# Optimization experiments

Hardware: AMD Instinct MI355X
Metric: run time of the kernel (lower is better)

Reference implementation:

```python
import jax, jax.numpy as jnp
import numpy as np

ANG = 5   # angular resolution (u = v = 5, n = 25 views)
CH = 64   # input channels
D = 2 * CH  # spa_dim + ang_dim + fre_dim = c/2 + c/2 + c = 128
NEG = -1e15


def _l2(x):
    # torch F.normalize over the contraction axis (last axis of folded layout)
    n = jnp.sqrt(jnp.sum(x * x, axis=-1, keepdims=True))
    return x / jnp.maximum(n, 1e-12)


def setup_inputs() -> dict:
    key = jax.random.key(0)
    ks = jax.random.split(key, 8)
    b, c, n, h, w = 4, CH, ANG * ANG, 32, 32
    d = D
    return {
        "x_lf": jax.random.normal(ks[0], (b, c, n, h, w), jnp.float32),
        "x_hf": jax.random.normal(ks[1], (b, c, n, h, w), jnp.float32),
        "W_in": jax.random.normal(ks[2], (c, d), jnp.float32) / np.sqrt(c).astype(np.float32),
        "W_kv": jax.random.normal(ks[3], (c, d), jnp.float32) / np.sqrt(c).astype(np.float32),
        "ln_g": jnp.ones((d,), jnp.float32),
        "ln_b": jnp.zeros((d,), jnp.float32),
        "W_m1": jax.random.normal(ks[4], (d, d), jnp.float32) / np.sqrt(d).astype(np.float32),
        "W_m2": jax.random.normal(ks[5], (d, d), jnp.float32) / np.sqrt(d).astype(np.float32),
        "W_out": jax.random.normal(ks[6], (d, c), jnp.float32) / np.sqrt(d).astype(np.float32),
    }


def _attend(fold, unfold, tq, tk, tv):
    # fold(t): (b, cc, u*v, h, w) -> (b, M, K); k/v use the same folding
    qf = _l2(fold(tq))            # q normalized over contraction axis
    kf = _l2(fold(tk))            # k normalized over contraction axis (dim=-2 of k^T)
    vf = fold(tv)
    att = jnp.einsum('bmk,bnk->bmn', qf, kf)   # (b, M, M)
    M = att.shape[-1]
    tril = jnp.tril(jnp.ones((M, M), bool))    # causal mask over folded axis
    att = jax.nn.softmax(jnp.where(tril, att, NEG), axis=-1)
    return unfold(att @ vf) + tv               # residual with token_v


def reference(x_lf, x_hf, W_in, W_kv, ln_g, ln_b, W_m1, W_m2, W_out):
    b, c, n, h, w = x_hf.shape
    u = v = ANG
    d = W_in.shape[1]

    def to_tokens(x, W):
        # 'b c (u v) h w -> (b u v) (h w) c' ; Linear ; back to 'b d (u v) h w'
        xt = x.reshape(b, c, u, v, h, w).transpose(0, 2, 3, 4, 5, 1).reshape(b * u * v, h * w, c)
        y = xt @ W
        return y.reshape(b, u, v, h, w, d).transpose(0, 5, 1, 2, 3, 4).reshape(b, d, u * v, h, w)

    q = to_tokens(x_hf, W_in)
    kv = to_tokens(x_lf, W_kv)
    cq = d // 4
    sf_q, af_q, sa_q = q[:, :cq], q[:, cq:2 * cq], q[:, 2 * cq:]
    sf_kv, af_kv, sa_kv = kv[:, :cq], kv[:, cq:2 * cq], kv[:, 2 * cq:]

    # SpatialFrequency: 'b c (u v) h w -> b (c h) (w u v)'
    def sf_fold(t):
        cc = t.shape[1]
        return t.reshape(b, cc, u, v, h, w).transpose(0, 1, 4, 5, 2, 3).reshape(b, cc * h, w * u * v)
    def sf_unfold(t):
        cc = t.shape[1] // h
        return t.reshape(b, cc, h, w, u, v).transpose(0, 1, 4, 5, 2, 3).reshape(b, cc, u * v, h, w)

    # AngularFrequency: 'b c (u v) h w -> b (c u) (h v w)'
    def af_fold(t):
        cc = t.shape[1]
        return t.reshape(b, cc, u, v, h, w).transpose(0, 1, 2, 4, 3, 5).reshape(b, cc * u, h * v * w)
    def af_unfold(t):
        cc = t.shape[1] // u
        return t.reshape(b, cc, u, h, v, w).transpose(0, 1, 2, 4, 3, 5).reshape(b, cc, u * v, h, w)

    # SpatialAngular: 'b c (u v) h w -> b (h u) (c v w)'
    def sa_fold(t):
        cc = t.shape[1]
        return t.reshape(b, cc, u, v, h, w).transpose(0, 4, 2, 1, 3, 5).reshape(b, h * u, cc * v * w)
    def sa_unfold(t):
        cc = t.shape[2] // (v * w) if t.ndim == 3 else t.shape[1]
        t = t.reshape(b, h, u, cc, v, w)
        return t.transpose(0, 3, 2, 4, 1, 5).reshape(b, cc, u * v, h, w)

    sf = _attend(sf_fold, sf_unfold, sf_q, sf_kv, sf_kv)
    af = _attend(af_fold, af_unfold, af_q, af_kv, af_kv)
    sa = _attend(sa_fold, sa_unfold, sa_q, sa_kv, sa_kv)

    cat = jnp.concatenate([sf, af, sa], axis=1)  # (b, d, n, h, w)
    ct = cat.reshape(b, d, u, v, h, w).transpose(0, 2, 3, 4, 5, 1).reshape(b * u * v, h * w, d)

    # c_mlp: LayerNorm -> Linear -> ReLU -> Linear (dropout is identity in eval)
    mu = jnp.mean(ct, axis=-1, keepdims=True)
    var = jnp.mean(jnp.square(ct - mu), axis=-1, keepdims=True)
    ln = (ct - mu) / jnp.sqrt(var + 1e-5) * ln_g + ln_b
    mlp = jax.nn.relu(ln @ W_m1) @ W_m2
    out_t = (mlp + ct) @ W_out  # residual then output projection

    out = out_t.reshape(b, u, v, h, w, -1).transpose(0, 5, 1, 2, 3, 4).reshape(b, -1, u * v, h, w)
    return out
```

## Files before the change

kernel.cpp:

```cpp
#include <hip/hip_runtime.h>

#define NSP   25600
#define HWC   1024

typedef __attribute__((ext_vector_type(8))) short bf8;
typedef __attribute__((ext_vector_type(4))) float f4;
#define MFMA(a,b,c) __builtin_amdgcn_mfma_f32_16x16x32_bf16(a, b, c, 0, 0, 0)
typedef unsigned short u16;

__device__ __forceinline__ u16 f2b(float f) {
    union { float f; unsigned u; } v; v.f = f;
    unsigned r = v.u + 0x7fffu + ((v.u >> 16) & 1u);
    return (u16)(r >> 16);
}
__device__ __forceinline__ float b2f(u16 h) {
    union { unsigned u; float f; } v; v.u = ((unsigned)h) << 16;
    return v.f;
}

__device__ __forceinline__ long row_base(int att, int b, int m) {
    if (att == 0) { int cc = m >> 5, h = m & 31;   return ((long)(b*128 + cc))*NSP + h*32; }
    else if (att == 1) { int cc = m / 5, u = m - cc*5; return ((long)(b*128 + 32 + cc))*NSP + u*5120; }
    else { int h = m / 5, u = m - h*5;            return ((long)(b*128 + 64))*NSP + u*5120 + h*32; }
}
__device__ __forceinline__ long chunk_off(int att, int kc) {
    if (att == 0) return (long)kc * 1024;
    else if (att == 1) return (long)kc * 32;
    else { int cc = kc / 5, v = kc - cc*5; return (long)cc*NSP + v*1024; }
}

__global__ __launch_bounds__(256) void k_prep(
        const float* __restrict__ Wi, const float* __restrict__ Wk,
        const float* __restrict__ W1, const float* __restrict__ W2,
        const float* __restrict__ Wo, u16* __restrict__ wbt) {
    int e = blockIdx.x * 256 + threadIdx.x;
    const float* src; int base, K, N;
    if (e < 8192)       { src = Wi; base = 0;     K = 64;  N = 128; }
    else if (e < 16384) { src = Wk; base = 8192;  K = 64;  N = 128; }
    else if (e < 32768) { src = W1; base = 16384; K = 128; N = 128; }
    else if (e < 49152) { src = W2; base = 32768; K = 128; N = 128; }
    else                { src = Wo; base = 49152; K = 128; N = 64;  }
    int local = e - base, n = local / K, k = local - n * K;
    wbt[e] = f2b(src[k * N + n]);
}

__global__ __launch_bounds__(256) void k_prep2(
        const float* __restrict__ W2, const float* __restrict__ Wo,
        u16* __restrict__ w2o) {
    int e = blockIdx.x * 256 + threadIdx.x;
    int o = e >> 7, k = e & 127;
    float s = 0.f;
    for (int n = 0; n < 128; ++n) s += W2[k * 128 + n] * Wo[n * 64 + o];
    w2o[e] = f2b(s);
}

__global__ __launch_bounds__(256) void k_tokens(
        const float* __restrict__ x_hf, const float* __restrict__ x_lf,
        const u16* __restrict__ wbt,
        u16* __restrict__ qb, u16* __restrict__ kvb) {
    int s0 = blockIdx.x * 64, b = blockIdx.y, which = blockIdx.z;
    const float* x  = which ? x_lf : x_hf;
    const u16* Wb = wbt + (which ? 8192 : 0);
    u16* out = which ? kvb : qb;
    __shared__ u16 Axs[64 * 72];
    __shared__ u16 Wl [128 * 72];
    int tid = threadIdx.x;
    for (int g = tid; g < 1024; g += 256) {
        int d = g >> 3, c8 = (g & 7) * 8;
        *(bf8*)&Wl[d * 72 + c8] = *(const bf8*)(Wb + d * 64 + c8);
    }
    for (int g = tid; g < 1024; g += 256) {
        int s = g & 63, c4 = (g >> 6) * 4;
        long xb = ((long)(b * 64 + c4)) * NSP + s0 + s;
        ushort4 pk;
        pk.x = f2b(x[xb]);
        pk.y = f2b(x[xb + NSP]);
        pk.z = f2b(x[xb + 2 * NSP]);
        pk.w = f2b(x[xb + 3 * NSP]);
        *(ushort4*)&Axs[s * 72 + c4] = pk;
    }
    __syncthreads();
    int w = tid >> 6, l = tid & 63, quad = l >> 4, col = l & 15;
    f4 z = {0.f, 0.f, 0.f, 0.f};
    f4 acc[8]; for (int i = 0; i < 8; ++i) acc[i] = z;
#pragma unroll
    for (int kc = 0; kc < 2; ++kc) {
        bf8 a = *(bf8*)&Axs[(w * 16 + col) * 72 + kc * 32 + quad * 8];
#pragma unroll
        for (int nt = 0; nt < 8; ++nt) {
            bf8 bb = *(bf8*)&Wl[(nt * 16 + col) * 72 + kc * 32 + quad * 8];
            acc[nt] = MFMA(a, bb, acc[nt]);
        }
    }
#pragma unroll
    for (int nt = 0; nt < 8; ++nt) {
        int d = nt * 16 + col;
        long base = ((long)(b * 128 + d)) * NSP + s0 + w * 16 + quad * 4;
        ushort4 pk;
        pk.x = f2b(acc[nt][0]); pk.y = f2b(acc[nt][1]);
        pk.z = f2b(acc[nt][2]); pk.w = f2b(acc[nt][3]);
        *(ushort4*)(out + base) = pk;
    }
}

__global__ __launch_bounds__(256) void k_vt_norms(
        const u16* __restrict__ qb, const u16* __restrict__ kvb,
        u16* __restrict__ vt0, u16* __restrict__ vt1, u16* __restrict__ vt2,
        float* __restrict__ nq, float* __restrict__ nk) {
    int x = blockIdx.x, b = blockIdx.y;
    int tid = threadIdx.x;
    __shared__ u16 T[128 * 36];
    if (x < 200) {
        int kc = x >> 3, pt = (x & 7) * 128;
        long co = (long)kc * 1024;
#pragma unroll
        for (int i = 0; i < 4; ++i) {
            int idx = i * 256 + tid;
            int r = idx >> 3, fq = (idx & 7) * 4;
            ushort4 e = *(const ushort4*)(kvb + row_base(0, b, pt + r) + co + fq);
            *(ushort4*)&T[r * 36 + fq] = e;
        }
        __syncthreads();
#pragma unroll
        for (int i = 0; i < 4; ++i) {
            int idx = i * 256 + tid;
            int f = idx >> 5, p4 = (idx & 31) * 4;
            ushort4 pk;
            pk.x = T[(p4    ) * 36 + f];
            pk.y = T[(p4 + 1) * 36 + f];
            pk.z = T[(p4 + 2) * 36 + f];
            pk.w = T[(p4 + 3) * 36 + f];
            *(ushort4*)(vt0 + (((long)b * 25 + kc) * 32 + f) * 1024 + pt + p4) = pk;
        }
    } else if (x < 2600) {
        int att, kc, pt, KC; u16* vt;
        if (x < 1000) { int x2 = x - 200;  att = 1; kc = x2 / 5; pt = (x2 - kc * 5) * 32; KC = 160; vt = vt1; }
        else          { int x3 = x - 1000; att = 2; kc = x3 / 5; pt = (x3 - kc * 5) * 32; KC = 320; vt = vt2; }
        long co = chunk_off(att, kc);
        {
            int r = tid >> 3, fq = (tid & 7) * 4;
            ushort4 e = *(const ushort4*)(kvb + row_base(att, b, pt + r) + co + fq);
            *(ushort4*)&T[r * 36 + fq] = e;
        }
        __syncthreads();
        {
            int f = tid >> 3, p4 = (tid & 7) * 4;
            ushort4 pk;
            pk.x = T[(p4    ) * 36 + f];
            pk.y = T[(p4 + 1) * 36 + f];
            pk.z = T[(p4 + 2) * 36 + f];
            pk.w = T[(p4 + 3) * 36 + f];
            *(ushort4*)(vt + (((long)b * KC + kc) * 32 + f) * 160 + pt + p4) = pk;
        }
    } else {
        int x2 = x - 2600;
        int which = x2 >= 336;
        int g = which ? x2 - 336 : x2;
        int att, m0, KC;
        if (g < 256)      { att = 0; m0 = g * 4;         KC = 25;  }
        else if (g < 296) { att = 1; m0 = (g - 256) * 4; KC = 160; }
        else              { att = 2; m0 = (g - 296) * 4; KC = 320; }
        const u16* src = which ? kvb : qb;
        float* dst = which ? nk : nq;
        int w = tid >> 6, lane = tid & 63;
        int m = m0 + w;
        long base = row_base(att, b, m);
        int K = KC * 32;
        float s = 0.f;
        for (int k8 = lane * 8; k8 < K; k8 += 512) {
            bf8 v = *(const bf8*)(src + base + chunk_off(att, k8 >> 5) + (k8 & 31));
#pragma unroll
            for (int j = 0; j < 8; ++j) { float f = b2f(((u16*)&v)[j]); s += f * f; }
        }
        for (int o = 32; o >= 1; o >>= 1) s += __shfl_xor(s, o);
        if (lane == 0) {
            int off = (att == 0) ? b * 1024 + m
                                 : ((att == 1) ? 4096 : 4736) + b * 160 + m;
            dst[off] = fmaxf(sqrtf(s), 1e-12f);
        }
    }
}

__global__ __launch_bounds__(256) void k_sgemm_all(
        const u16* __restrict__ qb, const u16* __restrict__ kvb,
        const float* __restrict__ nq, const float* __restrict__ nk,
        u16* __restrict__ Sb, float* __restrict__ Spart) {
    __shared__ float lds[4096];
    int x = blockIdx.x, b = blockIdx.y;
    int tid = threadIdx.x, w = tid >> 6, l = tid & 63, quad = l >> 4, col = l & 15;
    if (x < 136) {
        u16* Qs = (u16*)lds;
        u16* Ks = Qs + 64 * 40;
        int t = x, i = 0;
        while (t >= (i + 1) * (i + 2) / 2) ++i;
        int j = t - i * (i + 1) / 2;
        int mt = i * 64, nt = j * 64;
        int srow = tid >> 2, g = tid & 3;
        f4 z = {0.f, 0.f, 0.f, 0.f};
        f4 acc[4]; for (int q = 0; q < 4; ++q) acc[q] = z;
        for (int kc = 0; kc < 25; ++kc) {
            long co = (long)kc * 1024;
            {
                int m = mt + srow;
                *(bf8*)&Qs[srow * 40 + g * 8] =
                    *(const bf8*)(qb + ((long)(b*128 + (m >> 5)))*NSP + (m & 31)*32 + co + g*8);
                int n = nt + srow;
                *(bf8*)&Ks[srow * 40 + g * 8] =
                    *(const bf8*)(kvb + ((long)(b*128 + (n >> 5)))*NSP + (n & 31)*32 + co + g*8);
            }
            __syncthreads();
            bf8 a = *(bf8*)&Qs[(w * 16 + col) * 40 + quad * 8];
#pragma unroll
            for (int t2 = 0; t2 < 4; ++t2) {
                bf8 bb = *(bf8*)&Ks[(t2 * 16 + col) * 40 + quad * 8];
                acc[t2] = MFMA(a, bb, acc[t2]);
            }
            __syncthreads();
        }
#pragma unroll
        for (int t2 = 0; t2 < 4; ++t2)
#pragma unroll
            for (int r = 0; r < 4; ++r) {
                int m = mt + w * 16 + quad * 4 + r, n = nt + t2 * 16 + col;
                float v = (n <= m) ? acc[t2][r] / (nq[b*1024 + m] * nk[b*1024 + n]) : 0.f;
                Sb[((long)b * 1024 + m) * 1024 + n] = f2b(v);
            }
    } else {
        int x2 = x - 136;
        int t = x2 % 15, y = x2 / 15;
        int att, split, nsplit; float* base;
        if (y < 10) { att = 1; split = y;      nsplit = 10; base = Spart; }
        else        { att = 2; split = y - 10; nsplit = 20; base = Spart + 614400; }
        int i = 0;
        while (t >= (i + 1) * (i + 2) / 2) ++i;
        int j = t - i * (i + 1) / 2;
        int mt = i * 32, nt = j * 32;
        long rm0 = row_base(att, b, mt + col),      rm1 = row_base(att, b, mt + 16 + col);
        long rn0 = row_base(att, b, nt + col),      rn1 = row_base(att, b, nt + 16 + col);
        int ko = quad * 8;
        f4 z = {0.f, 0.f, 0.f, 0.f};
        f4 a00 = z, a01 = z, a10 = z, a11 = z;
#pragma unroll
        for (int s = 0; s < 4; ++s) {
            int kc = split * 16 + w * 4 + s;
            long co = chunk_off(att, kc);
            bf8 qa0 = *(const bf8*)(qb + rm0 + co + ko);
            bf8 qa1 = *(const bf8*)(qb + rm1 + co + ko);
            bf8 kb0 = *(const bf8*)(kvb + rn0 + co + ko);
            bf8 kb1 = *(const bf8*)(kvb + rn1 + co + ko);
            a00 = MFMA(qa0, kb0, a00); a01 = MFMA(qa0, kb1, a01);
            a10 = MFMA(qa1, kb0, a10); a11 = MFMA(qa1, kb1, a11);
        }
        float* my = lds + w * 1024;
#pragma unroll
        for (int r = 0; r < 4; ++r) {
            my[(quad * 4 + r) * 32 + col]            = a00[r];
            my[(quad * 4 + r) * 32 + 16 + col]       = a01[r];
            my[(16 + quad * 4 + r) * 32 + col]       = a10[r];
            my[(16 + quad * 4 + r) * 32 + 16 + col]  = a11[r];
        }
        __syncthreads();
        float* dst = base + ((long)((b * 15 + t) * nsplit + split)) * 1024;
        for (int e = tid; e < 1024; e += 256)
            dst[e] = lds[e] + lds[1024 + e] + lds[2048 + e] + lds[3072 + e];
    }
}

__global__ __launch_bounds__(256) void k_softmax_all(
        const u16* __restrict__ Sb, u16* __restrict__ Pb,
        const float* __restrict__ Spart, const float* __restrict__ nq,
        const float* __restrict__ nk, u16* __restrict__ Pb12) {
    int xb = blockIdx.x, b = blockIdx.y, tid = threadIdx.x;
    if (xb < 256) {
        int w = tid >> 6, lane = tid & 63;
        int m = xb * 4 + w;
        const u16* row = Sb + ((long)b * 1024 + m) * 1024;
        u16* pr = Pb + ((long)b * 1024 + m) * 1024;
        int e0 = lane * 16;
        bf8 x0 = *(const bf8*)(row + e0);
        bf8 x1 = *(const bf8*)(row + e0 + 8);
        float v[16];
#pragma unroll
        for (int j = 0; j < 8; ++j) { v[j] = b2f(((u16*)&x0)[j]); v[8 + j] = b2f(((u16*)&x1)[j]); }
        float mx = -1e30f;
#pragma unroll
        for (int j = 0; j < 16; ++j) if (e0 + j <= m) mx = fmaxf(mx, v[j]);
#pragma unroll
        for (int o = 32; o >= 1; o >>= 1) mx = fmaxf(mx, __shfl_xor(mx, o));
        float s = 0.f;
#pragma unroll
        for (int j = 0; j < 16; ++j) {
            float e = (e0 + j <= m) ? __expf(v[j] - mx) : 0.f;
            v[j] = e; s += e;
        }
#pragma unroll
        for (int o = 32; o >= 1; o >>= 1) s += __shfl_xor(s, o);
        float inv = 1.f / s;
        bf8 o0, o1;
#pragma unroll
        for (int j = 0; j < 8; ++j) {
            ((u16*)&o0)[j] = f2b(v[j] * inv);
            ((u16*)&o1)[j] = f2b(v[8 + j] * inv);
        }
        *(bf8*)(pr + e0) = o0;
        *(bf8*)(pr + e0 + 8) = o1;
    } else {
        int x = xb - 256;
        int att = (x < 160) ? 1 : 2;
        int m = (att == 1) ? x : x - 160;
        int nsplit = (att == 1) ? 10 : 20;
        const float* base = (att == 1) ? Spart : Spart + 614400;
        int noff = (att == 1) ? 4096 : 4736;
        u16* P = Pb12 + ((att == 1) ? 0 : 102400);
        int i = m >> 5, ro = (m & 31) * 32;
        int n = tid;
        bool act = (n <= m) && (n < 160);
        float myv = 0.f;
        if (act) {
            int t = i * (i + 1) / 2 + (n >> 5);
            const float* src = base + ((long)((b * 15 + t) * nsplit)) * 1024 + ro + (n & 31);
            float s = 0.f;
            for (int sp = 0; sp < nsplit; ++sp) s += src[(long)sp * 1024];
            myv = s / (nq[noff + b * 160 + m] * nk[noff + b * 160 + n]);
        }
        __shared__ float red[256];
        red[tid] = act ? myv : -1e30f; __syncthreads();
        for (int w = 128; w >= 1; w >>= 1) {
            if (tid < w) red[tid] = fmaxf(red[tid], red[tid + w]);
            __syncthreads();
        }
        float mx = red[0]; __syncthreads();
        float e = act ? __expf(myv - mx) : 0.f;
        red[tid] = e; __syncthreads();
        for (int w = 128; w >= 1; w >>= 1) {
            if (tid < w) red[tid] += red[tid + w];
            __syncthreads();
        }
        float inv = 1.f / red[0];
        if (n < 160) P[((long)b * 160 + m) * 160 + n] = f2b(e * inv);
    }
}

__global__ __launch_bounds__(256) void k_ogemm_all(
        const u16* __restrict__ Pb, const u16* __restrict__ vt0,
        const u16* __restrict__ Pb12, const u16* __restrict__ vt1,
        const u16* __restrict__ vt2, const u16* __restrict__ kvb,
        u16* __restrict__ catb) {
    __shared__ __align__(16) u16 lds[64 * 72 + 32 * 72];
    int x = blockIdx.x, b = blockIdx.y;
    int tid = threadIdx.x, w = tid >> 6, l = tid & 63, quad = l >> 4, col = l & 15;
    if (x < 400) {
        int mtt = x & 15, kc = x >> 4;
        int mt = mtt * 64;
        long co = (long)kc * 1024;
        const u16* vtc = vt0 + ((long)b * 25 + kc) * 32 * 1024;
        u16* Ps = lds;
        u16* Vs = lds + 64 * 72;
        f4 z = {0.f, 0.f, 0.f, 0.f};
        f4 acc[2]; acc[0] = z; acc[1] = z;
        for (int s = 0; s <= mtt; ++s) {
            int p0 = s * 64;
#pragma unroll
            for (int i = 0; i < 2; ++i) {
                int idx = i * 256 + tid;
                int row = idx >> 3, c8 = (idx & 7) * 8;
                *(bf8*)&Ps[row * 72 + c8] =
                    *(const bf8*)(Pb + ((long)(b * 1024 + mt + row)) * 1024 + p0 + c8);
            }
            {
                int f = tid >> 3, p8 = (tid & 7) * 8;
                *(bf8*)&Vs[f * 72 + p8] =
                    *(const bf8*)(vtc + (long)f * 1024 + p0 + p8);
            }
            __syncthreads();
            bf8 a0 = *(bf8*)&Ps[(w * 16 + col) * 72 + quad * 8];
            bf8 a1 = *(bf8*)&Ps[(w * 16 + col) * 72 + 32 + quad * 8];
#pragma unroll
            for (int t2 = 0; t2 < 2; ++t2) {
                bf8 b0 = *(bf8*)&Vs[(t2 * 16 + col) * 72 + quad * 8];
                bf8 b1 = *(bf8*)&Vs[(t2 * 16 + col) * 72 + 32 + quad * 8];
                acc[t2] = MFMA(a0, b0, acc[t2]);
                acc[t2] = MFMA(a1, b1, acc[t2]);
            }
            __syncthreads();
        }
#pragma unroll
        for (int t2 = 0; t2 < 2; ++t2)
#pragma unroll
            for (int r = 0; r < 4; ++r) {
                int m = mt + w * 16 + quad * 4 + r, f = t2 * 16 + col;
                long adr = ((long)(b * 128 + (m >> 5))) * NSP + (m & 31) * 32 + co + f;
                catb[adr] = f2b(acc[t2][r] + b2f(kvb[adr]));
            }
    } else {
        int x2 = x - 400;
        int att = (x2 < 320) ? 1 : 2;
        int ft  = (att == 1) ? x2 : x2 - 320;
        int KC  = (att == 1) ? 160 : 320;
        const u16* vt = (att == 1) ? vt1 : vt2;
        const u16* Prow = Pb12 + ((att == 1) ? 0 : 102400) + (long)b * 160 * 160;
        u16* Vs = lds;
        for (int g = tid; g < 320; g += 256) {
            int fl = g / 20, p8 = (g % 20) * 8;
            int fglob = ft * 16 + fl;
            int kc = fglob >> 5, fr = fglob & 31;
            *(bf8*)&Vs[fl * 168 + p8] =
                *(const bf8*)(vt + (((long)b * KC + kc) * 32 + fr) * 160 + p8);
        }
        __syncthreads();
        int fglob = ft * 16 + col;
        int kcf = fglob >> 5, fi = fglob & 31;
        long cbase = chunk_off(att, kcf) + fi;
        f4 z = {0.f, 0.f, 0.f, 0.f};
        for (int j = 0; j < 3; ++j) {
            int mi = w + 4 * j;
            if (mi >= 10) break;
            int nkk = (mi >> 1) + 1;
            f4 acc = z;
#pragma unroll 5
            for (int kk = 0; kk < nkk; ++kk) {
                bf8 a  = *(const bf8*)(Prow + (mi * 16 + col) * 160 + kk * 32 + quad * 8);
                bf8 bb = *(bf8*)&Vs[col * 168 + kk * 32 + quad * 8];
                acc = MFMA(a, bb, acc);
            }
#pragma unroll
            for (int r = 0; r < 4; ++r) {
                int m = mi * 16 + quad * 4 + r;
                long adr = row_base(att, b, m) + cbase;
                catb[adr] = f2b(acc[r] + b2f(kvb[adr]));
            }
        }
    }
}

__global__ __launch_bounds__(256) void k_mlp_fused(
        const u16* __restrict__ catb, const float* __restrict__ g,
        const float* __restrict__ be, const u16* __restrict__ wbt,
        const u16* __restrict__ w2o, float* __restrict__ out) {
    int x = blockIdx.x, tid = threadIdx.x;
    int tt = x * 64;
    int bn = tt >> 10, hwt = tt & 1023;
    int b = bn / 25, uv = bn - b * 25;
    __shared__ u16 CT[64 * 136];
    __shared__ u16 Wt[128 * 136];
    __shared__ float gl[128], bl[128], mu_s[64], rs_s[64];
    int w = tid >> 6, l = tid & 63, quad = l >> 4, col = l & 15;
    const u16* src = catb + (long)b * 128 * NSP + (long)uv * HWC + hwt;
#pragma unroll
    for (int i = 0; i < 4; ++i) {
        int gi = i * 256 + tid;
        int d = gi >> 3, hw8 = (gi & 7) * 8;
        bf8 v = *(const bf8*)(src + (long)d * NSP + hw8);
#pragma unroll
        for (int j = 0; j < 8; ++j) CT[(hw8 + j) * 136 + d] = ((u16*)&v)[j];
    }
    {
        const u16* Wob = wbt + 49152;
        for (int q = tid; q < 1024; q += 256) {
            int o = q >> 4, k8 = (q & 15) * 8;
            *(bf8*)&Wt[o * 136 + k8] = *(const bf8*)(Wob + o * 128 + k8);
        }
    }
    if (tid < 128) { gl[tid] = g[tid]; bl[tid] = be[tid]; }
    __syncthreads();
    f4 z = {0.f, 0.f, 0.f, 0.f};
    f4 acc_o[4]; for (int i = 0; i < 4; ++i) acc_o[i] = z;
#pragma unroll
    for (int kc = 0; kc < 4; ++kc) {
        bf8 a = *(bf8*)&CT[(w * 16 + col) * 136 + kc * 32 + quad * 8];
#pragma unroll
        for (int nt = 0; nt < 4; ++nt) {
            bf8 bb = *(bf8*)&Wt[(nt * 16 + col) * 136 + kc * 32 + quad * 8];
            acc_o[nt] = MFMA(a, bb, acc_o[nt]);
        }
    }
    {
        int tk = w * 16 + (l >> 2), dg = (l & 3) * 32;
        float s = 0.f, s2 = 0.f;
#pragma unroll
        for (int q = 0; q < 4; ++q) {
            bf8 vv = *(bf8*)&CT[tk * 136 + dg + q * 8];
#pragma unroll
            for (int j = 0; j < 8; ++j) { float f = b2f(((u16*)&vv)[j]); s += f; s2 += f * f; }
        }
        s += __shfl_xor(s, 1); s2 += __shfl_xor(s2, 1);
        s += __shfl_xor(s, 2); s2 += __shfl_xor(s2, 2);
        if ((l & 3) == 0) {
            float m = s * (1.f / 128.f);
            float var = s2 * (1.f / 128.f) - m * m;
            mu_s[tk] = m; rs_s[tk] = rsqrtf(var + 1e-5f);
        }
    }
    __syncthreads();
    for (int q = tid; q < 1024; q += 256) {
        int row = q >> 4, k8 = (q & 15) * 8;
        bf8 cv = *(bf8*)&CT[row * 136 + k8];
        float m = mu_s[row], rs = rs_s[row];
        bf8 av;
#pragma unroll
        for (int j = 0; j < 8; ++j)
            ((u16*)&av)[j] = f2b((b2f(((u16*)&cv)[j]) - m) * rs * gl[k8 + j] + bl[k8 + j]);
        *(bf8*)&CT[row * 136 + k8] = av;
    }
    {
        const u16* W1b = wbt + 16384;
        for (int q = tid; q < 2048; q += 256) {
            int n = q >> 4, k8 = (q & 15) * 8;
            *(bf8*)&Wt[n * 136 + k8] = *(const bf8*)(W1b + n * 128 + k8);
        }
    }
    __syncthreads();
    f4 acc_h[8]; for (int i = 0; i < 8; ++i) acc_h[i] = z;
#pragma unroll
    for (int kc = 0; kc < 4; ++kc) {
        bf8 a = *(bf8*)&CT[(w * 16 + col) * 136 + kc * 32 + quad * 8];
#pragma unroll
        for (int nt = 0; nt < 8; ++nt) {
            bf8 bb = *(bf8*)&Wt[(nt * 16 + col) * 136 + kc * 32 + quad * 8];
            acc_h[nt] = MFMA(a, bb, acc_h[nt]);
        }
    }
    __syncthreads();
#pragma unroll
    for (int nt = 0; nt < 8; ++nt)
#pragma unroll
        for (int r = 0; r < 4; ++r) {
            int row = w * 16 + quad * 4 + r, n = nt * 16 + col;
            CT[row * 136 + n] = f2b(fmaxf(acc_h[nt][r], 0.f));
        }
    for (int q = tid; q < 1024; q += 256) {
        int o = q >> 4, k8 = (q & 15) * 8;
        *(bf8*)&Wt[o * 136 + k8] = *(const bf8*)(w2o + o * 128 + k8);
    }
    __syncthreads();
#pragma unroll
    for (int kc = 0; kc < 4; ++kc) {
        bf8 a = *(bf8*)&CT[(w * 16 + col) * 136 + kc * 32 + quad * 8];
#pragma unroll
        for (int nt = 0; nt < 4; ++nt) {
            bf8 bb = *(bf8*)&Wt[(nt * 16 + col) * 136 + kc * 32 + quad * 8];
            acc_o[nt] = MFMA(a, bb, acc_o[nt]);
        }
    }
    int hw = hwt + w * 16 + quad * 4;
#pragma unroll
    for (int nt = 0; nt < 4; ++nt) {
        int o = nt * 16 + col;
        float4 pk = {acc_o[nt][0], acc_o[nt][1], acc_o[nt][2], acc_o[nt][3]};
        *(float4*)(out + ((long)((b * 64 + o) * 25 + uv)) * 1024 + hw) = pk;
    }
}

extern "C" void kernel_launch(void* const* d_in, const int* in_sizes, int n_in,
                              void* d_out, int out_size, void* d_ws, size_t ws_size,
                              hipStream_t stream) {
    const float* x_lf = (const float*)d_in[0];
    const float* x_hf = (const float*)d_in[1];
    const float* W_in = (const float*)d_in[2];
    const float* W_kv = (const float*)d_in[3];
    const float* ln_g = (const float*)d_in[4];
    const float* ln_b = (const float*)d_in[5];
    const float* W_m1 = (const float*)d_in[6];
    const float* W_m2 = (const float*)d_in[7];
    const float* W_ot = (const float*)d_in[8];
    float* out = (float*)d_out;

    float* ws = (float*)d_ws;
    u16*   qb    = (u16*)ws;
    u16*   kvb   = (u16*)(ws + 6553600);
    u16*   catb  = (u16*)(ws + 13107200);
    u16*   Sb    = (u16*)(ws + 26214400);
    u16*   Pb    = (u16*)(ws + 28311552);
    u16*   Pb12  = (u16*)(ws + 30408704);
    float* Spart = ws + 30511104;
    float* nq    = ws + 32354304;
    float* nk    = ws + 32359680;
    u16*   w2ob  = (u16*)(ws + 32365056);
    u16*   vt0   = (u16*)(ws + 32569856);
    u16*   vt1   = (u16*)(ws + 34208256);
    u16*   vt2   = (u16*)(ws + 35846656);
    u16*   wbt   = (u16*)(ws + 39123456);

    k_prep<<<dim3(224), 256, 0, stream>>>(W_in, W_kv, W_m1, W_m2, W_ot, wbt);
    k_prep2<<<dim3(32), 256, 0, stream>>>(W_m2, W_ot, w2ob);

    k_tokens<<<dim3(400, 4, 2), 256, 0, stream>>>(x_hf, x_lf, wbt, qb, kvb);

    k_vt_norms<<<dim3(3272, 4), 256, 0, stream>>>(qb, kvb, vt0, vt1, vt2, nq, nk);

    k_sgemm_all<<<dim3(586, 4), 256, 0, stream>>>(qb, kvb, nq, nk, Sb, Spart);

    k_softmax_all<<<dim3(576, 4), 256, 0, stream>>>(Sb, Pb, Spart, nq, nk, Pb12);

    k_ogemm_all<<<dim3(1360, 4), 256, 0, stream>>>(Pb, vt0, Pb12, vt1, vt2, kvb, catb);

    k_mlp_fused<<<dim3(1600), 256, 0, stream>>>(catb, ln_g, ln_b, wbt, w2ob, out);
}
```

Baseline: 275.5 us.

## Merge V-transpose and norm kernel into score GEMM, defer normalization to softmax

The separate V-transpose/norm kernel is folded into the score GEMM launch as extra block ranges, removing one launch and letting the independent work overlap. Because the GEMM no longer waits for the norms, it writes unscaled dot products. The norm blocks store reciprocal norms, and the softmax kernel applies them as multiplications. The sf-path GEMM also stages two K-chunks per LDS round, halving the barriers, and hoists the row-address math. The risk is that unnormalized scores are rounded to bf16 before scaling, which changes precision slightly.

```diff
diff --git a/kernel.cpp b/kernel.cpp
--- a/kernel.cpp
+++ b/kernel.cpp
@@ -103,117 +103,52 @@
     }
 }
 
-__global__ __launch_bounds__(256) void k_vt_norms(
+__global__ __launch_bounds__(256) void k_sgemm_all(
         const u16* __restrict__ qb, const u16* __restrict__ kvb,
         u16* __restrict__ vt0, u16* __restrict__ vt1, u16* __restrict__ vt2,
-        float* __restrict__ nq, float* __restrict__ nk) {
-    int x = blockIdx.x, b = blockIdx.y;
-    int tid = threadIdx.x;
-    __shared__ u16 T[128 * 36];
-    if (x < 200) {
-        int kc = x >> 3, pt = (x & 7) * 128;
-        long co = (long)kc * 1024;
-#pragma unroll
-        for (int i = 0; i < 4; ++i) {
-            int idx = i * 256 + tid;
-            int r = idx >> 3, fq = (idx & 7) * 4;
-            ushort4 e = *(const ushort4*)(kvb + row_base(0, b, pt + r) + co + fq);
-            *(ushort4*)&T[r * 36 + fq] = e;
-        }
-        __syncthreads();
-#pragma unroll
-        for (int i = 0; i < 4; ++i) {
-            int idx = i * 256 + tid;
-            int f = idx >> 5, p4 = (idx & 31) * 4;
-            ushort4 pk;
-            pk.x = T[(p4    ) * 36 + f];
-            pk.y = T[(p4 + 1) * 36 + f];
-            pk.z = T[(p4 + 2) * 36 + f];
-            pk.w = T[(p4 + 3) * 36 + f];
-            *(ushort4*)(vt0 + (((long)b * 25 + kc) * 32 + f) * 1024 + pt + p4) = pk;
-        }
-    } else if (x < 2600) {
-        int att, kc, pt, KC; u16* vt;
-        if (x < 1000) { int x2 = x - 200;  att = 1; kc = x2 / 5; pt = (x2 - kc * 5) * 32; KC = 160; vt = vt1; }
-        else          { int x3 = x - 1000; att = 2; kc = x3 / 5; pt = (x3 - kc * 5) * 32; KC = 320; vt = vt2; }
-        long co = chunk_off(att, kc);
-        {
-            int r = tid >> 3, fq = (tid & 7) * 4;
-            ushort4 e = *(const ushort4*)(kvb + row_base(att, b, pt + r) + co + fq);
-            *(ushort4*)&T[r * 36 + fq] = e;
-        }
-        __syncthreads();
-        {
-            int f = tid >> 3, p4 = (tid & 7) * 4;
-            ushort4 pk;
-            pk.x = T[(p4    ) * 36 + f];
-            pk.y = T[(p4 + 1) * 36 + f];
-            pk.z = T[(p4 + 2) * 36 + f];
-            pk.w = T[(p4 + 3) * 36 + f];
-            *(ushort4*)(vt + (((long)b * KC + kc) * 32 + f) * 160 + pt + p4) = pk;
-        }
-    } else {
-        int x2 = x - 2600;
-        int which = x2 >= 336;
-        int g = which ? x2 - 336 : x2;
-        int att, m0, KC;
-        if (g < 256)      { att = 0; m0 = g * 4;         KC = 25;  }
-        else if (g < 296) { att = 1; m0 = (g - 256) * 4; KC = 160; }
-        else              { att = 2; m0 = (g - 296) * 4; KC = 320; }
-        const u16* src = which ? kvb : qb;
-        float* dst = which ? nk : nq;
-        int w = tid >> 6, lane = tid & 63;
-        int m = m0 + w;
-        long base = row_base(att, b, m);
-        int K = KC * 32;
-        float s = 0.f;
-        for (int k8 = lane * 8; k8 < K; k8 += 512) {
-            bf8 v = *(const bf8*)(src + base + chunk_off(att, k8 >> 5) + (k8 & 31));
-#pragma unroll
-            for (int j = 0; j < 8; ++j) { float f = b2f(((u16*)&v)[j]); s += f * f; }
-        }
-        for (int o = 32; o >= 1; o >>= 1) s += __shfl_xor(s, o);
-        if (lane == 0) {
-            int off = (att == 0) ? b * 1024 + m
-                                 : ((att == 1) ? 4096 : 4736) + b * 160 + m;
-            dst[off] = fmaxf(sqrtf(s), 1e-12f);
-        }
-    }
-}
-
-__global__ __launch_bounds__(256) void k_sgemm_all(
-        const u16* __restrict__ qb, const u16* __restrict__ kvb,
-        const float* __restrict__ nq, const float* __restrict__ nk,
+        float* __restrict__ nq, float* __restrict__ nk,
         u16* __restrict__ Sb, float* __restrict__ Spart) {
-    __shared__ float lds[4096];
+    __shared__ __align__(16) u16 lds[2 * 64 * 72];
     int x = blockIdx.x, b = blockIdx.y;
     int tid = threadIdx.x, w = tid >> 6, l = tid & 63, quad = l >> 4, col = l & 15;
     if (x < 136) {
-        u16* Qs = (u16*)lds;
-        u16* Ks = Qs + 64 * 40;
+        u16* Qs = lds;
+        u16* Ks = lds + 64 * 72;
         int t = x, i = 0;
         while (t >= (i + 1) * (i + 2) / 2) ++i;
         int j = t - i * (i + 1) / 2;
         int mt = i * 64, nt = j * 64;
         int srow = tid >> 2, g = tid & 3;
+        int mr = mt + srow, nr = nt + srow;
+        long qrow = ((long)(b * 128 + (mr >> 5))) * NSP + (mr & 31) * 32;
+        long krow = ((long)(b * 128 + (nr >> 5))) * NSP + (nr & 31) * 32;
         f4 z = {0.f, 0.f, 0.f, 0.f};
         f4 acc[4]; for (int q = 0; q < 4; ++q) acc[q] = z;
-        for (int kc = 0; kc < 25; ++kc) {
+        for (int kc = 0; kc < 25; kc += 2) {
             long co = (long)kc * 1024;
-            {
-                int m = mt + srow;
-                *(bf8*)&Qs[srow * 40 + g * 8] =
-                    *(const bf8*)(qb + ((long)(b*128 + (m >> 5)))*NSP + (m & 31)*32 + co + g*8);
-                int n = nt + srow;
-                *(bf8*)&Ks[srow * 40 + g * 8] =
-                    *(const bf8*)(kvb + ((long)(b*128 + (n >> 5)))*NSP + (n & 31)*32 + co + g*8);
+            bool two = (kc + 1 < 25);
+            *(bf8*)&Qs[srow * 72 + g * 8] = *(const bf8*)(qb + qrow + co + g * 8);
+            *(bf8*)&Ks[srow * 72 + g * 8] = *(const bf8*)(kvb + krow + co + g * 8);
+            if (two) {
+                *(bf8*)&Qs[srow * 72 + 32 + g * 8] =
+                    *(const bf8*)(qb + qrow + co + 1024 + g * 8);
+                *(bf8*)&Ks[srow * 72 + 32 + g * 8] =
+                    *(const bf8*)(kvb + krow + co + 1024 + g * 8);
             }
             __syncthreads();
-            bf8 a = *(bf8*)&Qs[(w * 16 + col) * 40 + quad * 8];
+            bf8 a0 = *(bf8*)&Qs[(w * 16 + col) * 72 + quad * 8];
 #pragma unroll
             for (int t2 = 0; t2 < 4; ++t2) {
-                bf8 bb = *(bf8*)&Ks[(t2 * 16 + col) * 40 + quad * 8];
-                acc[t2] = MFMA(a, bb, acc[t2]);
+                bf8 bb = *(bf8*)&Ks[(t2 * 16 + col) * 72 + quad * 8];
+                acc[t2] = MFMA(a0, bb, acc[t2]);
+            }
+            if (two) {
+                bf8 a1 = *(bf8*)&Qs[(w * 16 + col) * 72 + 32 + quad * 8];
+#pragma unroll
+                for (int t2 = 0; t2 < 4; ++t2) {
+                    bf8 bb = *(bf8*)&Ks[(t2 * 16 + col) * 72 + 32 + quad * 8];
+                    acc[t2] = MFMA(a1, bb, acc[t2]);
+                }
             }
             __syncthreads();
         }
@@ -222,10 +157,11 @@
 #pragma unroll
             for (int r = 0; r < 4; ++r) {
                 int m = mt + w * 16 + quad * 4 + r, n = nt + t2 * 16 + col;
-                float v = (n <= m) ? acc[t2][r] / (nq[b*1024 + m] * nk[b*1024 + n]) : 0.f;
+                float v = (n <= m) ? acc[t2][r] : 0.f;
                 Sb[((long)b * 1024 + m) * 1024 + n] = f2b(v);
             }
-    } else {
+    } else if (x < 586) {
+        float* fl = (float*)lds;
         int x2 = x - 136;
         int t = x2 % 15, y = x2 / 15;
         int att, split, nsplit; float* base;
@@ -251,7 +187,7 @@
             a00 = MFMA(qa0, kb0, a00); a01 = MFMA(qa0, kb1, a01);
             a10 = MFMA(qa1, kb0, a10); a11 = MFMA(qa1, kb1, a11);
         }
-        float* my = lds + w * 1024;
+        float* my = fl + w * 1024;
 #pragma unroll
         for (int r = 0; r < 4; ++r) {
             my[(quad * 4 + r) * 32 + col]            = a00[r];
@@ -262,7 +198,78 @@
         __syncthreads();
         float* dst = base + ((long)((b * 15 + t) * nsplit + split)) * 1024;
         for (int e = tid; e < 1024; e += 256)
-            dst[e] = lds[e] + lds[1024 + e] + lds[2048 + e] + lds[3072 + e];
+            dst[e] = fl[e] + fl[1024 + e] + fl[2048 + e] + fl[3072 + e];
+    } else if (x < 786) {
+        u16* T = lds;
+        int xv = x - 586;
+        int kc = xv >> 3, pt = (xv & 7) * 128;
+        long co = (long)kc * 1024;
+#pragma unroll
+        for (int i = 0; i < 4; ++i) {
+            int idx = i * 256 + tid;
+            int r = idx >> 3, fq = (idx & 7) * 4;
+            ushort4 e = *(const ushort4*)(kvb + row_base(0, b, pt + r) + co + fq);
+            *(ushort4*)&T[r * 36 + fq] = e;
+        }
+        __syncthreads();
+#pragma unroll
+        for (int i = 0; i < 4; ++i) {
+            int idx = i * 256 + tid;
+            int f = idx >> 5, p4 = (idx & 31) * 4;
+            ushort4 pk;
+            pk.x = T[(p4    ) * 36 + f];
+            pk.y = T[(p4 + 1) * 36 + f];
+            pk.z = T[(p4 + 2) * 36 + f];
+            pk.w = T[(p4 + 3) * 36 + f];
+            *(ushort4*)(vt0 + (((long)b * 25 + kc) * 32 + f) * 1024 + pt + p4) = pk;
+        }
+    } else if (x < 3186) {
+        u16* T = lds;
+        int att, kc, pt, KC; u16* vt;
+        if (x < 1586) { int y = x - 786;  att = 1; kc = y / 5;  pt = (y - kc * 5) * 32;  KC = 160; vt = vt1; }
+        else          { int y = x - 1586; att = 2; kc = y / 5;  pt = (y - kc * 5) * 32;  KC = 320; vt = vt2; }
+        long co = chunk_off(att, kc);
+        {
+            int r = tid >> 3, fq = (tid & 7) * 4;
+            ushort4 e = *(const ushort4*)(kvb + row_base(att, b, pt + r) + co + fq);
+            *(ushort4*)&T[r * 36 + fq] = e;
+        }
+        __syncthreads();
+        {
+            int f = tid >> 3, p4 = (tid & 7) * 4;
+            ushort4 pk;
+            pk.x = T[(p4    ) * 36 + f];
+            pk.y = T[(p4 + 1) * 36 + f];
+            pk.z = T[(p4 + 2) * 36 + f];
+            pk.w = T[(p4 + 3) * 36 + f];
+            *(ushort4*)(vt + (((long)b * KC + kc) * 32 + f) * 160 + pt + p4) = pk;
+        }
+    } else {
+        int x2 = x - 3186;
+        int which = x2 >= 336;
+        int g = which ? x2 - 336 : x2;
+        int att, m0, KC;
+        if (g < 256)      { att = 0; m0 = g * 4;         KC = 25;  }
+        else if (g < 296) { att = 1; m0 = (g - 256) * 4; KC = 160; }
+        else              { att = 2; m0 = (g - 296) * 4; KC = 320; }
+        const u16* src = which ? kvb : qb;
+        float* dst = which ? nk : nq;
+        int ww = tid >> 6, lane = tid & 63;
+        int m = m0 + ww;
+        long base = row_base(att, b, m);
+        int K = KC * 32;
+        float s = 0.f;
+        for (int k8 = lane * 8; k8 < K; k8 += 512) {
+            bf8 v = *(const bf8*)(src + base + chunk_off(att, k8 >> 5) + (k8 & 31));
+#pragma unroll
+            for (int j = 0; j < 8; ++j) { float f = b2f(((u16*)&v)[j]); s += f * f; }
+        }
+        for (int o = 32; o >= 1; o >>= 1) s += __shfl_xor(s, o);
+        if (lane == 0) {
+            int off = (att == 0) ? b * 1024 + m
+                                 : ((att == 1) ? 4096 : 4736) + b * 160 + m;
+            dst[off] = 1.f / fmaxf(sqrtf(s), 1e-12f);
+        }
     }
 }
 
@@ -277,11 +284,21 @@
         const u16* row = Sb + ((long)b * 1024 + m) * 1024;
         u16* pr = Pb + ((long)b * 1024 + m) * 1024;
         int e0 = lane * 16;
+        float rq = nq[b * 1024 + m];
+        const float* nkb = nk + b * 1024 + e0;
+        float rk[16];
+        *(float4*)&rk[0]  = *(const float4*)(nkb);
+        *(float4*)&rk[4]  = *(const float4*)(nkb + 4);
+        *(float4*)&rk[8]  = *(const float4*)(nkb + 8);
+        *(float4*)&rk[12] = *(const float4*)(nkb + 12);
         bf8 x0 = *(const bf8*)(row + e0);
         bf8 x1 = *(const bf8*)(row + e0 + 8);
         float v[16];
 #pragma unroll
-        for (int j = 0; j < 8; ++j) { v[j] = b2f(((u16*)&x0)[j]); v[8 + j] = b2f(((u16*)&x1)[j]); }
+        for (int j = 0; j < 8; ++j) {
+            v[j]     = b2f(((u16*)&x0)[j]) * rq * rk[j];
+            v[8 + j] = b2f(((u16*)&x1)[j]) * rq * rk[8 + j];
+        }
         float mx = -1e30f;
 #pragma unroll
         for (int j = 0; j < 16; ++j) if (e0 + j <= m) mx = fmaxf(mx, v[j]);
@@ -321,7 +338,7 @@
             const float* src = base + ((long)((b * 15 + t) * nsplit)) * 1024 + ro + (n & 31);
             float s = 0.f;
             for (int sp = 0; sp < nsplit; ++sp) s += src[(long)sp * 1024];
-            myv = s / (nq[noff + b * 160 + m] * nk[noff + b * 160 + n]);
+            myv = s * (nq[noff + b * 160 + m] * nk[noff + b * 160 + n]);
         }
         __shared__ float red[256];
         red[tid] = act ? myv : -1e30f; __syncthreads();
@@ -586,9 +603,8 @@
 
     k_tokens<<<dim3(400, 4, 2), 256, 0, stream>>>(x_hf, x_lf, wbt, qb, kvb);
 
-    k_vt_norms<<<dim3(3272, 4), 256, 0, stream>>>(qb, kvb, vt0, vt1, vt2, nq, nk);
-
-    k_sgemm_all<<<dim3(586, 4), 256, 0, stream>>>(qb, kvb, nq, nk, Sb, Spart);
+    k_sgemm_all<<<dim3(3858, 4), 256, 0, stream>>>(qb, kvb, vt0, vt1, vt2,
+                                                   nq, nk, Sb, Spart);
 
     k_softmax_all<<<dim3(576, 4), 256, 0, stream>>>(Sb, Pb, Spart, nq, nk, Pb12);
 
```

Result: faster. 267.1 us (-3.1%).
